# Kernel tuning notes

Measured on AMD Instinct MI355X. Metric: run time of the kernel, lower is better.

Reference implementation:

```python
import jax, jax.numpy as jnp
import numpy as np
from jax import lax

# dims
B, H, W, C = 32, 64, 64, 256
FEATURES, HEADS, NQ = 256, 8, 2
K, STRIDE, PAD = 3, 2, 1
HD = FEATURES // HEADS  # head dim = 32


def setup_inputs() -> dict:
    key = jax.random.key(0)
    ks = jax.random.split(key, 7)
    x = jax.random.normal(ks[0], (B, H, W, C), jnp.float32)
    # learned shared queries: truncated normal * sqrt(1/head_dim)
    query = jax.random.truncated_normal(ks[1], -2.0, 2.0, (NQ, FEATURES), jnp.float32) * np.float32(np.sqrt(1.0 / HD))
    Wk = jax.random.normal(ks[2], (C, FEATURES), jnp.float32) * np.float32(np.sqrt(1.0 / C))  # lecun
    Wv = jax.random.normal(ks[3], (C, FEATURES), jnp.float32) * np.float32(np.sqrt(1.0 / C))
    rpe_bias = jax.random.truncated_normal(ks[4], -2.0, 2.0, (K * K, NQ * HEADS), jnp.float32) * np.float32(0.02)
    attn_scale_w = jax.random.normal(ks[5], (K * K, NQ * HEADS), jnp.float32) * np.float32(0.02)
    Wo = jax.random.normal(ks[6], (FEATURES, FEATURES), jnp.float32) * np.float32(np.sqrt(1.0 / FEATURES))
    return {"x": x, "query": query, "Wk": Wk, "Wv": Wv,
            "rpe_bias": rpe_bias, "attn_scale_w": attn_scale_w, "Wo": Wo}


def _qna_forward(x, query, Wk, Wv, rpe_bias, attn_scale_w, Wo):
    # --- queries: reshape to [NQ, HEADS, HD], unit-normalize per head, depth-scale ---
    q = query.reshape(NQ, HEADS, HD)
    q = q / (jnp.linalg.norm(q, axis=-1, keepdims=True) + 1e-6)
    q = q / jnp.sqrt(HD).astype(q.dtype)

    # --- fused QK: (q Wk^T) applied to x, never materializing per-window keys ---
    Wk_r = Wk.reshape(C, HEADS, HD)
    qWk = jnp.einsum('qHd,DHd->DqH', q, Wk_r)              # [C, NQ, HEADS]
    cost = jnp.einsum('bijD,DqH->bijqH', x, qWk)            # [B, H, W, NQ, HEADS]
    cost_exp = jnp.exp(cost - lax.stop_gradient(jnp.max(cost)))  # global shift, cancels in softmax

    # --- values ---
    v = jnp.einsum('bijD,DF->bijF', x, Wv)                  # [B, H, W, FEATURES]
    v_cost_exp = cost_exp[..., None] * v.reshape(B, H, W, 1, HEADS, HD)
    v_cost_exp = v_cost_exp.reshape(B, H, W, NQ * FEATURES)

    # --- relative position bias + per-offset query mixing scale ---
    rpe = rpe_bias.reshape(K, K, 1, NQ * HEADS)
    rpe_exp = jnp.exp(rpe - lax.stop_gradient(jnp.max(rpe)))  # shift cancels (appears in num & den)
    scale = attn_scale_w.reshape(K, K, 1, NQ * HEADS)
    num_kernel = jnp.repeat(rpe_exp * scale, HD, axis=-1)   # [K, K, 1, NQ*FEATURES]

    # numerator: windowed sum of exp(cost)*v weighted by exp(rpe)*scale (depthwise conv)
    num = lax.conv_general_dilated(
        v_cost_exp, num_kernel, window_strides=(STRIDE, STRIDE),
        padding=((PAD, PAD), (PAD, PAD)), feature_group_count=NQ * FEATURES,
        dimension_numbers=('NHWC', 'HWIO', 'NHWC'))
    # denominator: windowed sum of exp(cost) weighted by exp(rpe)
    den = lax.conv_general_dilated(
        cost_exp.reshape(B, H, W, NQ * HEADS), rpe_exp, window_strides=(STRIDE, STRIDE),
        padding=((PAD, PAD), (PAD, PAD)), feature_group_count=NQ * HEADS,
        dimension_numbers=('NHWC', 'HWIO', 'NHWC'))
    ho, wo = num.shape[1], num.shape[2]

    out = num.reshape(B, ho, wo, NQ, HEADS, HD) / den.reshape(B, ho, wo, NQ, HEADS, 1)
    out = out.sum(axis=3).reshape(B, ho, wo, FEATURES)      # combine queries
    return jnp.einsum('bijF,FO->bijO', out, Wo)             # output projection


def reference(x, query, Wk, Wv, rpe_bias, attn_scale_w, Wo):
    return _qna_forward(x, query, Wk, Wv, rpe_bias, attn_scale_w, Wo)
```

## Files before the change

### kernel.cpp

```cpp
#include <hip/hip_runtime.h>
#include <math.h>

typedef __attribute__((ext_vector_type(8))) short bf16x8;
typedef __attribute__((ext_vector_type(4))) float floatx4;

static __device__ __forceinline__ short f2bf(float f) {
    union { float f; unsigned u; } a; a.f = f;
    unsigned r = a.u + 0x7fffu + ((a.u >> 16) & 1u);
    return (short)(r >> 16);
}
static __device__ __forceinline__ float bf2f(short s) {
    union { unsigned u; float f; } c; c.u = ((unsigned)(unsigned short)s) << 16;
    return c.f;
}

__global__ __launch_bounds__(256) void prep_kernel(
    const float* __restrict__ query,
    const float* __restrict__ Wk,
    const float* __restrict__ rpe_bias,
    const float* __restrict__ attn_scale_w,
    const float* __restrict__ Wv,
    const float* __restrict__ Wo,
    float* __restrict__ rpe_exp,
    float* __restrict__ rpe_scale,
    short* __restrict__ Bq,
    short* __restrict__ Wvh,
    short* __restrict__ Bo)
{
    __shared__ float qn[16 * 33];
    __shared__ float Wt[16][260];
    __shared__ float qwk_s[16][17];
    int tid = threadIdx.x, bb = blockIdx.x;

    for (int i = tid; i < 512; i += 256) {
        int qq  = i >> 8;
        int rem = i & 255;
        int h   = rem >> 5;
        int d   = rem & 31;
        qn[((qq << 3) + h) * 33 + d] = query[i];
    }
    for (int i = tid; i < 16 * 256; i += 256)
        Wt[i >> 8][i & 255] = Wk[bb * 16 * 256 + i];
    __syncthreads();
    if (tid < 16) {
        float s = 0.f;
        #pragma unroll
        for (int d = 0; d < 32; ++d) { float t = qn[tid * 33 + d]; s += t * t; }
        float inv = 1.0f / ((sqrtf(s) + 1e-6f) * sqrtf(32.0f));
        #pragma unroll
        for (int d = 0; d < 32; ++d) qn[tid * 33 + d] *= inv;
    }
    __syncthreads();

    int g  = tid & 15;
    int Dl = tid >> 4;
    int h2 = g & 7;
    float acc = 0.f;
    #pragma unroll
    for (int d = 0; d < 32; ++d)
        acc += qn[g * 33 + d] * Wt[Dl][h2 * 32 + d];
    qwk_s[Dl][g] = acc;
    __syncthreads();

    {
        int kl = tid >> 4, gg = tid & 15;
        int k  = bb * 16 + kl;
        int kc = k >> 5, q5 = k & 31, qd = q5 >> 3, j = q5 & 7;
        int lane = qd * 16 + gg;
        Bq[kc * 512 + lane * 8 + j] = f2bf(qwk_s[kl][gg]);
    }

    for (int kl = 0; kl < 16; ++kl) {
        int k  = bb * 16 + kl;
        int kc = k >> 5, q5 = k & 31, qd = q5 >> 3, j = q5 & 7;
        int n  = tid;
        int gg = n & 15;
        int lane = qd * 16 + gg;
        float vv = Wv[k * 256 + n];
        float vo = Wo[k * 256 + n];
        int nt  = n >> 4;
        Wvh[nt * 4096 + kc * 512 + lane * 8 + j] = f2bf(vv);
        Bo[nt * 4096 + kc * 512 + lane * 8 + j]  = f2bf(vo);
    }

    if (bb == 0 && tid < 144) {
        float r = expf(rpe_bias[tid]);
        rpe_exp[tid]   = r;
        rpe_scale[tid] = r * attn_scale_w[tid];
    }
}

#define XROW 264
#define CESROW 19
__global__ __launch_bounds__(512) void fused_kernel(
    const float* __restrict__ x,
    const float* __restrict__ rpe_exp,
    const float* __restrict__ rpe_scale,
    const short* __restrict__ Bq,
    const short* __restrict__ Wvh,
    const short* __restrict__ Bo,
    float* __restrict__ out)
{
    __shared__ short Xw[112 * XROW];
    __shared__ __align__(16) unsigned char pool[112 * CESROW * 4];
    __shared__ float wcoefs[8][9][16];
    __shared__ float invden[16][16];

    float* ces    = (float*)pool;
    short* out_tr = (short*)pool;

    int tid  = threadIdx.x;
    int lane = tid & 63, wv = tid >> 6;
    int m16  = lane & 15, quad = lane >> 4;

    int blk0 = blockIdx.x;
    int blk  = ((blk0 & 7) << 8) | (blk0 >> 3);
    int b   = blk >> 6;
    int io  = (blk >> 1) & 31;
    int hf  = blk & 1;
    int i0  = io * 2 - 1;
    int jbase = hf * 32 - 1;

    #pragma unroll
    for (int i = 0; i < 7; ++i) {
        int it  = tid + i * 512;
        int row = it >> 5;
        int l   = it & 31;
        int ky  = row / 34;
        int jloc = row - ky * 34;
        int ii = i0 + ky, jj = jbase + jloc;
        bool valid = (ky < 3) && (jloc < 33) &&
                     ((unsigned)ii < 64u) && ((unsigned)jj < 64u);
        bf16x8 s;
        if (valid) {
            const float* xp = x + ((size_t)(((b << 6) + ii) << 6) + jj) * 256 + l * 8;
            float4 f0 = *(const float4*)xp;
            float4 f1 = *(const float4*)(xp + 4);
            s[0] = f2bf(f0.x); s[1] = f2bf(f0.y); s[2] = f2bf(f0.z); s[3] = f2bf(f0.w);
            s[4] = f2bf(f1.x); s[5] = f2bf(f1.y); s[6] = f2bf(f1.z); s[7] = f2bf(f1.w);
        } else {
            #pragma unroll
            for (int j = 0; j < 8; ++j) s[j] = 0;
        }
        *(bf16x8*)&Xw[row * XROW + l * 8] = s;
    }
    __syncthreads();

    if (wv < 7) {
        bf16x8 Arow[8];
        const short* xrow = &Xw[(wv * 16 + m16) * XROW + quad * 8];
        #pragma unroll
        for (int kc = 0; kc < 8; ++kc)
            Arow[kc] = *(const bf16x8*)(xrow + kc * 32);

        floatx4 accc = (floatx4){0.f, 0.f, 0.f, 0.f};
        const short* bq = Bq + lane * 8;
        #pragma unroll
        for (int kc = 0; kc < 8; ++kc)
            accc = __builtin_amdgcn_mfma_f32_16x16x32_bf16(
                       Arow[kc], *(const bf16x8*)(bq + kc * 512), accc, 0, 0, 0);
        #pragma unroll
        for (int r = 0; r < 4; ++r) {
            int p = wv * 16 + quad * 4 + r;
            int ky = p / 34, jloc = p - ky * 34;
            int ii = i0 + ky, jj = jbase + jloc;
            bool valid = (ky < 3) && (jloc < 33) &&
                         ((unsigned)ii < 64u) && ((unsigned)jj < 64u);
            ces[p * CESROW + m16] = valid ? expf(accc[r]) : 0.f;
        }

        const short* bv = Wvh + lane * 8;
        #pragma unroll
        for (int ntp = 0; ntp < 8; ++ntp) {
            floatx4 a0 = (floatx4){0.f, 0.f, 0.f, 0.f};
            floatx4 a1 = (floatx4){0.f, 0.f, 0.f, 0.f};
            const short* bp0 = bv + (2 * ntp) * 4096;
            #pragma unroll
            for (int kc = 0; kc < 8; ++kc) {
                bf16x8 b0 = *(const bf16x8*)(bp0 + kc * 512);
                bf16x8 b1 = *(const bf16x8*)(bp0 + 4096 + kc * 512);
                a0 = __builtin_amdgcn_mfma_f32_16x16x32_bf16(Arow[kc], b0, a0, 0, 0, 0);
                a1 = __builtin_amdgcn_mfma_f32_16x16x32_bf16(Arow[kc], b1, a1, 0, 0, 0);
            }
            #pragma unroll
            for (int r = 0; r < 4; ++r) {
                Xw[(wv * 16 + quad * 4 + r) * XROW + ntp * 32 + m16]      = f2bf(a0[r]);
                Xw[(wv * 16 + quad * 4 + r) * XROW + ntp * 32 + 16 + m16] = f2bf(a1[r]);
            }
        }
    }
    __syncthreads();

    if (tid < 256) {
        int op = tid >> 4, g = tid & 15;
        float den = 0.f;
        #pragma unroll
        for (int w = 0; w < 9; ++w) {
            int ky = w / 3, kx = w - ky * 3;
            int row = ky * 34 + 2 * op + kx;
            den = fmaf(rpe_exp[w * 16 + g], ces[row * CESROW + g], den);
        }
        invden[op][g] = 1.0f / den;
    }
    __syncthreads();

    for (int it = tid; it < 1152; it += 512) {
        int op = it / 72, r = it - op * 72;
        int w = r >> 3, h = r & 7;
        int ky = w / 3, kx = w - ky * 3;
        int row = ky * 34 + 2 * op + kx;
        wcoefs[h][w][op] =
            ces[row * CESROW + h]     * rpe_scale[w * 16 + h]     * invden[op][h] +
            ces[row * CESROW + 8 + h] * rpe_scale[w * 16 + 8 + h] * invden[op][8 + h];
    }
    __syncthreads();

    {
        int op = tid >> 5;
        int nc = tid & 31;
        int n0 = nc * 8;
        int h  = nc >> 2;
        float wcv[9];
        #pragma unroll
        for (int w = 0; w < 9; ++w) wcv[w] = wcoefs[h][w][op];

        float o[8];
        #pragma unroll
        for (int j = 0; j < 8; ++j) o[j] = 0.f;
        #pragma unroll
        for (int w = 0; w < 9; ++w) {
            int ky = w / 3, kx = w - ky * 3;
            int row = ky * 34 + 2 * op + kx;
            bf16x8 vv = *(const bf16x8*)&Xw[row * XROW + n0];
            #pragma unroll
            for (int j = 0; j < 8; ++j)
                o[j] = fmaf(wcv[w], bf2f(vv[j]), o[j]);
        }
        bf16x8 ob;
        #pragma unroll
        for (int j = 0; j < 8; ++j) ob[j] = f2bf(o[j]);
        *(bf16x8*)&out_tr[op * XROW + n0] = ob;
    }
    __syncthreads();

    {
        floatx4 acc0 = (floatx4){0.f, 0.f, 0.f, 0.f};
        floatx4 acc1 = (floatx4){0.f, 0.f, 0.f, 0.f};
        int nt0 = wv * 2;
        const short* bp = Bo + nt0 * 4096 + lane * 8;
        #pragma unroll
        for (int kc = 0; kc < 8; ++kc) {
            bf16x8 a  = *(const bf16x8*)&out_tr[m16 * XROW + kc * 32 + quad * 8];
            bf16x8 b0 = *(const bf16x8*)(bp + kc * 512);
            bf16x8 b1 = *(const bf16x8*)(bp + 4096 + kc * 512);
            acc0 = __builtin_amdgcn_mfma_f32_16x16x32_bf16(a, b0, acc0, 0, 0, 0);
            acc1 = __builtin_amdgcn_mfma_f32_16x16x32_bf16(a, b1, acc1, 0, 0, 0);
        }
        size_t op0 = (size_t)blk * 16;
        #pragma unroll
        for (int r = 0; r < 4; ++r) {
            out[(op0 + quad * 4 + r) * 256 + nt0 * 16 + m16]       = acc0[r];
            out[(op0 + quad * 4 + r) * 256 + (nt0 + 1) * 16 + m16] = acc1[r];
        }
    }
}

extern "C" void kernel_launch(void* const* d_in, const int* in_sizes, int n_in,
                              void* d_out, int out_size, void* d_ws, size_t ws_size,
                              hipStream_t stream)
{
    const float* x     = (const float*)d_in[0];
    const float* query = (const float*)d_in[1];
    const float* Wk    = (const float*)d_in[2];
    const float* Wv    = (const float*)d_in[3];
    const float* rpe   = (const float*)d_in[4];
    const float* asw   = (const float*)d_in[5];
    const float* Wo    = (const float*)d_in[6];
    float* out = (float*)d_out;

    float* ws        = (float*)d_ws;
    float* rpe_exp   = ws;
    float* rpe_scale = ws + 144;
    short* Bq        = (short*)(ws + 288);
    short* Wvh       = (short*)(ws + 288 + 2048);
    short* Bo        = (short*)(ws + 288 + 2048 + 32768);

    prep_kernel<<<dim3(16), dim3(256), 0, stream>>>(query, Wk, rpe, asw, Wv, Wo,
                                                    rpe_exp, rpe_scale, Bq, Wvh, Bo);
    fused_kernel<<<dim3(2048), dim3(512), 0, stream>>>(x, rpe_exp, rpe_scale,
                                                       Bq, Wvh, Bo, out);
}
```

Before: 306.6 us.

## Repartition V projection so each wave holds a Wv column slice in registers

The value-projection MFMA loop is restructured so each of the 8 waves keeps one 32-column slice of Wv in registers and loops over all 7 row tiles of the window, instead of each of 7 waves streaming all of Wv for its own row tile. This cuts repeated global/L2 loads of Wv per block and puts the eighth wave to work. In exchange it adds a __syncthreads per row tile so results can be written back into the shared X buffer in place, and it raises register pressure from the 16 resident B fragments.

```diff
diff --git a/kernel.cpp b/kernel.cpp
--- a/kernel.cpp
+++ b/kernel.cpp
@@ -146,19 +146,26 @@
     }
     __syncthreads();
 
+    bf16x8 Bv0[8], Bv1[8];
+    {
+        const short* bv = Wvh + (2 * wv) * 4096 + lane * 8;
+        #pragma unroll
+        for (int kc = 0; kc < 8; ++kc) {
+            Bv0[kc] = *(const bf16x8*)(bv + kc * 512);
+            Bv1[kc] = *(const bf16x8*)(bv + 4096 + kc * 512);
+        }
+    }
+
     if (wv < 7) {
-        bf16x8 Arow[8];
+        floatx4 accc = (floatx4){0.f, 0.f, 0.f, 0.f};
+        const short* bq   = Bq + lane * 8;
         const short* xrow = &Xw[(wv * 16 + m16) * XROW + quad * 8];
         #pragma unroll
-        for (int kc = 0; kc < 8; ++kc)
-            Arow[kc] = *(const bf16x8*)(xrow + kc * 32);
-
-        floatx4 accc = (floatx4){0.f, 0.f, 0.f, 0.f};
-        const short* bq = Bq + lane * 8;
-        #pragma unroll
-        for (int kc = 0; kc < 8; ++kc)
+        for (int kc = 0; kc < 8; ++kc) {
+            bf16x8 a = *(const bf16x8*)(xrow + kc * 32);
             accc = __builtin_amdgcn_mfma_f32_16x16x32_bf16(
-                       Arow[kc], *(const bf16x8*)(bq + kc * 512), accc, 0, 0, 0);
+                       a, *(const bf16x8*)(bq + kc * 512), accc, 0, 0, 0);
+        }
         #pragma unroll
         for (int r = 0; r < 4; ++r) {
             int p = wv * 16 + quad * 4 + r;
@@ -168,29 +175,27 @@
                          ((unsigned)ii < 64u) && ((unsigned)jj < 64u);
             ces[p * CESROW + m16] = valid ? expf(accc[r]) : 0.f;
         }
-
-        const short* bv = Wvh + lane * 8;
-        #pragma unroll
-        for (int ntp = 0; ntp < 8; ++ntp) {
-            floatx4 a0 = (floatx4){0.f, 0.f, 0.f, 0.f};
-            floatx4 a1 = (floatx4){0.f, 0.f, 0.f, 0.f};
-            const short* bp0 = bv + (2 * ntp) * 4096;
-            #pragma unroll
-            for (int kc = 0; kc < 8; ++kc) {
-                bf16x8 b0 = *(const bf16x8*)(bp0 + kc * 512);
-                bf16x8 b1 = *(const bf16x8*)(bp0 + 4096 + kc * 512);
-                a0 = __builtin_amdgcn_mfma_f32_16x16x32_bf16(Arow[kc], b0, a0, 0, 0, 0);
-                a1 = __builtin_amdgcn_mfma_f32_16x16x32_bf16(Arow[kc], b1, a1, 0, 0, 0);
-            }
-            #pragma unroll
-            for (int r = 0; r < 4; ++r) {
-                Xw[(wv * 16 + quad * 4 + r) * XROW + ntp * 32 + m16]      = f2bf(a0[r]);
-                Xw[(wv * 16 + quad * 4 + r) * XROW + ntp * 32 + 16 + m16] = f2bf(a1[r]);
-            }
-        }
-    }
-    __syncthreads();
-
+    }
+
+    for (int m = 0; m < 7; ++m) {
+        floatx4 a0 = (floatx4){0.f, 0.f, 0.f, 0.f};
+        floatx4 a1 = (floatx4){0.f, 0.f, 0.f, 0.f};
+        const short* xrow = &Xw[(m * 16 + m16) * XROW + quad * 8];
+        #pragma unroll
+        for (int kc = 0; kc < 8; ++kc) {
+            bf16x8 af = *(const bf16x8*)(xrow + kc * 32);
+            a0 = __builtin_amdgcn_mfma_f32_16x16x32_bf16(af, Bv0[kc], a0, 0, 0, 0);
+            a1 = __builtin_amdgcn_mfma_f32_16x16x32_bf16(af, Bv1[kc], a1, 0, 0, 0);
+        }
+        __syncthreads();
+        #pragma unroll
+        for (int r = 0; r < 4; ++r) {
+            Xw[(m * 16 + quad * 4 + r) * XROW + wv * 32 + m16]      = f2bf(a0[r]);
+            Xw[(m * 16 + quad * 4 + r) * XROW + wv * 32 + 16 + m16] = f2bf(a1[r]);
+        }
+    }
+
+    __syncthreads();
     if (tid < 256) {
         int op = tid >> 4, g = tid & 15;
         float den = 0.f;
```

Result: faster. 257.4 us (-16.0%).

## Split fused kernel into value projection pass and windowed attention pass

Applied to the files above, without the earlier changes.

Splits the single fused kernel into two. The first computes bf16 values and exp(cost) once per input pixel and stores them in a global workspace. The second reads them to form the windowed softmax numerator and denominator and the output projection. This removes the overlapping-halo recomputation of the value projection and the repeated loads of x. In exchange it adds a global round trip of the V and cost tensors, one extra launch, and a much larger workspace requirement.

```diff
diff --git a/kernel.cpp b/kernel.cpp
--- a/kernel.cpp
+++ b/kernel.cpp
@@ -90,24 +90,88 @@
     }
 }
 
-#define XROW 264
-#define CESROW 19
-__global__ __launch_bounds__(512) void fused_kernel(
+#define XROWA 264
+__global__ __launch_bounds__(256) void va_kernel(
     const float* __restrict__ x,
+    const short* __restrict__ Bq,
+    const short* __restrict__ Wvh,
+    short* __restrict__ V,
+    float* __restrict__ cesg)
+{
+    __shared__ short XA[64 * XROWA];
+    int tid  = threadIdx.x;
+    int lane = tid & 63, wv = tid >> 6;
+    int m16  = lane & 15, quad = lane >> 4;
+    size_t p0 = (size_t)blockIdx.x * 64;
+
+    #pragma unroll
+    for (int i = 0; i < 8; ++i) {
+        int it  = tid + i * 256;
+        int row = it >> 5, l = it & 31;
+        const float* xp = x + (p0 + row) * 256 + l * 8;
+        float4 f0 = *(const float4*)xp;
+        float4 f1 = *(const float4*)(xp + 4);
+        bf16x8 s;
+        s[0] = f2bf(f0.x); s[1] = f2bf(f0.y); s[2] = f2bf(f0.z); s[3] = f2bf(f0.w);
+        s[4] = f2bf(f1.x); s[5] = f2bf(f1.y); s[6] = f2bf(f1.z); s[7] = f2bf(f1.w);
+        *(bf16x8*)&XA[row * XROWA + l * 8] = s;
+    }
+    __syncthreads();
+
+    bf16x8 Arow[8];
+    const short* xrow = &XA[(wv * 16 + m16) * XROWA + quad * 8];
+    #pragma unroll
+    for (int kc = 0; kc < 8; ++kc)
+        Arow[kc] = *(const bf16x8*)(xrow + kc * 32);
+    __syncthreads();
+
+    {
+        floatx4 acc = (floatx4){0.f, 0.f, 0.f, 0.f};
+        const short* bq = Bq + lane * 8;
+        #pragma unroll
+        for (int kc = 0; kc < 8; ++kc)
+            acc = __builtin_amdgcn_mfma_f32_16x16x32_bf16(
+                      Arow[kc], *(const bf16x8*)(bq + kc * 512), acc, 0, 0, 0);
+        #pragma unroll
+        for (int r = 0; r < 4; ++r)
+            cesg[(p0 + wv * 16 + quad * 4 + r) * 16 + m16] = expf(acc[r]);
+    }
+
+    #pragma unroll 4
+    for (int nt = 0; nt < 16; ++nt) {
+        floatx4 acc = (floatx4){0.f, 0.f, 0.f, 0.f};
+        const short* bp = Wvh + nt * 4096 + lane * 8;
+        #pragma unroll
+        for (int kc = 0; kc < 8; ++kc)
+            acc = __builtin_amdgcn_mfma_f32_16x16x32_bf16(
+                      Arow[kc], *(const bf16x8*)(bp + kc * 512), acc, 0, 0, 0);
+        #pragma unroll
+        for (int r = 0; r < 4; ++r)
+            XA[(wv * 16 + quad * 4 + r) * XROWA + nt * 16 + m16] = f2bf(acc[r]);
+    }
+    __syncthreads();
+
+    #pragma unroll
+    for (int i = 0; i < 8; ++i) {
+        int it  = tid + i * 256;
+        int row = it >> 5, l = it & 31;
+        *(bf16x8*)&V[(p0 + row) * 256 + l * 8] =
+            *(const bf16x8*)&XA[row * XROWA + l * 8];
+    }
+}
+
+#define OROW 264
+__global__ __launch_bounds__(512) void qb_kernel(
+    const float* __restrict__ cesg,
+    const short* __restrict__ V,
     const float* __restrict__ rpe_exp,
     const float* __restrict__ rpe_scale,
-    const short* __restrict__ Bq,
-    const short* __restrict__ Wvh,
     const short* __restrict__ Bo,
     float* __restrict__ out)
 {
-    __shared__ short Xw[112 * XROW];
-    __shared__ __align__(16) unsigned char pool[112 * CESROW * 4];
+    __shared__ short out_tr[16 * OROW];
     __shared__ float wcoefs[8][9][16];
     __shared__ float invden[16][16];
-
-    float* ces    = (float*)pool;
-    short* out_tr = (short*)pool;
 
     int tid  = threadIdx.x;
     int lane = tid & 63, wv = tid >> 6;
@@ -121,84 +185,17 @@
     int i0  = io * 2 - 1;
     int jbase = hf * 32 - 1;
 
-    #pragma unroll
-    for (int i = 0; i < 7; ++i) {
-        int it  = tid + i * 512;
-        int row = it >> 5;
-        int l   = it & 31;
-        int ky  = row / 34;
-        int jloc = row - ky * 34;
-        int ii = i0 + ky, jj = jbase + jloc;
-        bool valid = (ky < 3) && (jloc < 33) &&
-                     ((unsigned)ii < 64u) && ((unsigned)jj < 64u);
-        bf16x8 s;
-        if (valid) {
-            const float* xp = x + ((size_t)(((b << 6) + ii) << 6) + jj) * 256 + l * 8;
-            float4 f0 = *(const float4*)xp;
-            float4 f1 = *(const float4*)(xp + 4);
-            s[0] = f2bf(f0.x); s[1] = f2bf(f0.y); s[2] = f2bf(f0.z); s[3] = f2bf(f0.w);
-            s[4] = f2bf(f1.x); s[5] = f2bf(f1.y); s[6] = f2bf(f1.z); s[7] = f2bf(f1.w);
-        } else {
-            #pragma unroll
-            for (int j = 0; j < 8; ++j) s[j] = 0;
-        }
-        *(bf16x8*)&Xw[row * XROW + l * 8] = s;
-    }
-    __syncthreads();
-
-    if (wv < 7) {
-        bf16x8 Arow[8];
-        const short* xrow = &Xw[(wv * 16 + m16) * XROW + quad * 8];
-        #pragma unroll
-        for (int kc = 0; kc < 8; ++kc)
-            Arow[kc] = *(const bf16x8*)(xrow + kc * 32);
-
-        floatx4 accc = (floatx4){0.f, 0.f, 0.f, 0.f};
-        const short* bq = Bq + lane * 8;
-        #pragma unroll
-        for (int kc = 0; kc < 8; ++kc)
-            accc = __builtin_amdgcn_mfma_f32_16x16x32_bf16(
-                       Arow[kc], *(const bf16x8*)(bq + kc * 512), accc, 0, 0, 0);
-        #pragma unroll
-        for (int r = 0; r < 4; ++r) {
-            int p = wv * 16 + quad * 4 + r;
-            int ky = p / 34, jloc = p - ky * 34;
-            int ii = i0 + ky, jj = jbase + jloc;
-            bool valid = (ky < 3) && (jloc < 33) &&
-                         ((unsigned)ii < 64u) && ((unsigned)jj < 64u);
-            ces[p * CESROW + m16] = valid ? expf(accc[r]) : 0.f;
-        }
-
-        const short* bv = Wvh + lane * 8;
-        #pragma unroll
-        for (int ntp = 0; ntp < 8; ++ntp) {
-            floatx4 a0 = (floatx4){0.f, 0.f, 0.f, 0.f};
-            floatx4 a1 = (floatx4){0.f, 0.f, 0.f, 0.f};
-            const short* bp0 = bv + (2 * ntp) * 4096;
-            #pragma unroll
-            for (int kc = 0; kc < 8; ++kc) {
-                bf16x8 b0 = *(const bf16x8*)(bp0 + kc * 512);
-                bf16x8 b1 = *(const bf16x8*)(bp0 + 4096 + kc * 512);
-                a0 = __builtin_amdgcn_mfma_f32_16x16x32_bf16(Arow[kc], b0, a0, 0, 0, 0);
-                a1 = __builtin_amdgcn_mfma_f32_16x16x32_bf16(Arow[kc], b1, a1, 0, 0, 0);
-            }
-            #pragma unroll
-            for (int r = 0; r < 4; ++r) {
-                Xw[(wv * 16 + quad * 4 + r) * XROW + ntp * 32 + m16]      = f2bf(a0[r]);
-                Xw[(wv * 16 + quad * 4 + r) * XROW + ntp * 32 + 16 + m16] = f2bf(a1[r]);
-            }
-        }
-    }
-    __syncthreads();
-
     if (tid < 256) {
         int op = tid >> 4, g = tid & 15;
         float den = 0.f;
         #pragma unroll
         for (int w = 0; w < 9; ++w) {
             int ky = w / 3, kx = w - ky * 3;
-            int row = ky * 34 + 2 * op + kx;
-            den = fmaf(rpe_exp[w * 16 + g], ces[row * CESROW + g], den);
+            int ii = i0 + ky, jj = jbase + 2 * op + kx;
+            if ((unsigned)ii < 64u && (unsigned)jj < 64u) {
+                size_t pix = ((size_t)((b << 6) + ii) << 6) + jj;
+                den = fmaf(rpe_exp[w * 16 + g], cesg[pix * 16 + g], den);
+            }
         }
         invden[op][g] = 1.0f / den;
     }
@@ -208,17 +205,20 @@
         int op = it / 72, r = it - op * 72;
         int w = r >> 3, h = r & 7;
         int ky = w / 3, kx = w - ky * 3;
-        int row = ky * 34 + 2 * op + kx;
-        wcoefs[h][w][op] =
-            ces[row * CESROW + h]     * rpe_scale[w * 16 + h]     * invden[op][h] +
-            ces[row * CESROW + 8 + h] * rpe_scale[w * 16 + 8 + h] * invden[op][8 + h];
+        int ii = i0 + ky, jj = jbase + 2 * op + kx;
+        float v = 0.f;
+        if ((unsigned)ii < 64u && (unsigned)jj < 64u) {
+            size_t pix = ((size_t)((b << 6) + ii) << 6) + jj;
+            v = cesg[pix * 16 + h]     * rpe_scale[w * 16 + h]     * invden[op][h] +
+                cesg[pix * 16 + 8 + h] * rpe_scale[w * 16 + 8 + h] * invden[op][8 + h];
+        }
+        wcoefs[h][w][op] = v;
     }
     __syncthreads();
 
     {
         int op = tid >> 5;
         int nc = tid & 31;
-        int n0 = nc * 8;
         int h  = nc >> 2;
         float wcv[9];
         #pragma unroll
@@ -230,8 +230,10 @@
         #pragma unroll
         for (int w = 0; w < 9; ++w) {
             int ky = w / 3, kx = w - ky * 3;
-            int row = ky * 34 + 2 * op + kx;
-            bf16x8 vv = *(const bf16x8*)&Xw[row * XROW + n0];
+            int ii = i0 + ky, jj = jbase + 2 * op + kx;
+            bool valid = ((unsigned)ii < 64u) && ((unsigned)jj < 64u);
+            size_t pix = valid ? (((size_t)((b << 6) + ii) << 6) + jj) : 0;
+            bf16x8 vv = *(const bf16x8*)&V[pix * 256 + nc * 8];
             #pragma unroll
             for (int j = 0; j < 8; ++j)
                 o[j] = fmaf(wcv[w], bf2f(vv[j]), o[j]);
@@ -239,7 +241,7 @@
         bf16x8 ob;
         #pragma unroll
         for (int j = 0; j < 8; ++j) ob[j] = f2bf(o[j]);
-        *(bf16x8*)&out_tr[op * XROW + n0] = ob;
+        *(bf16x8*)&out_tr[op * OROW + nc * 8] = ob;
     }
     __syncthreads();
 
@@ -250,7 +252,7 @@
         const short* bp = Bo + nt0 * 4096 + lane * 8;
         #pragma unroll
         for (int kc = 0; kc < 8; ++kc) {
-            bf16x8 a  = *(const bf16x8*)&out_tr[m16 * XROW + kc * 32 + quad * 8];
+            bf16x8 a  = *(const bf16x8*)&out_tr[m16 * OROW + kc * 32 + quad * 8];
             bf16x8 b0 = *(const bf16x8*)(bp + kc * 512);
             bf16x8 b1 = *(const bf16x8*)(bp + 4096 + kc * 512);
             acc0 = __builtin_amdgcn_mfma_f32_16x16x32_bf16(a, b0, acc0, 0, 0, 0);
@@ -284,9 +286,12 @@
     short* Bq        = (short*)(ws + 288);
     short* Wvh       = (short*)(ws + 288 + 2048);
     short* Bo        = (short*)(ws + 288 + 2048 + 32768);
+    short* V         = (short*)(ws + 68608);
+    float* cesg      = ws + 68608 + 16777216;
 
     prep_kernel<<<dim3(16), dim3(256), 0, stream>>>(query, Wk, rpe, asw, Wv, Wo,
                                                     rpe_exp, rpe_scale, Bq, Wvh, Bo);
-    fused_kernel<<<dim3(2048), dim3(512), 0, stream>>>(x, rpe_exp, rpe_scale,
-                                                       Bq, Wvh, Bo, out);
-}
+    va_kernel<<<dim3(2048), dim3(256), 0, stream>>>(x, Bq, Wvh, V, cesg);
+    qb_kernel<<<dim3(2048), dim3(512), 0, stream>>>(cesg, V, rpe_exp, rpe_scale,
+                                                    Bo, out);
+}
```

After: 289.2 us. 1.06x faster.
